# Performance work log

Measured on AMD Instinct MI355X. Metric: run time of the kernel, lower is better.

The kernel has to match this reference:

```python
import jax, jax.numpy as jnp
import numpy as np
from jax import lax

DILATIONS = [1, 2, 4, 8, 16, 32, 64, 128, 256, 512] * 2  # 20 layers
C = 128   # residual channels
K = 2     # kernel size


def _causal_dilated_conv(x, w, b, d):
    # x: [B, C, T], w: [2C, C, K], left-pad by d*(K-1) for causality
    pad = d * (K - 1)
    y = lax.conv_general_dilated(
        x, w, window_strides=(1,), padding=[(pad, 0)],
        rhs_dilation=(d,), dimension_numbers=('NCH', 'OIH', 'NCH'))
    return y + b[None, :, None]


def setup_inputs() -> dict:
    key = jax.random.key(0)
    ks = jax.random.split(key, 5)
    L = len(DILATIONS)
    x = jax.random.normal(ks[0], (4, C, 8192), jnp.float32)
    # 0.05 scale keeps activations stable through 20 residual layers
    w_conv = jax.random.normal(ks[1], (L, 2 * C, C, K), jnp.float32) * 0.05
    b_conv = jax.random.normal(ks[2], (L, 2 * C), jnp.float32) * 0.05
    w_out = jax.random.normal(ks[3], (L, C, C), jnp.float32) * 0.05
    b_out = jax.random.normal(ks[4], (L, C), jnp.float32) * 0.05
    return {"x": x, "w_conv": w_conv, "b_conv": b_conv,
            "w_out": w_out, "b_out": b_out}


def reference(x, w_conv, b_conv, w_out, b_out):
    """WaveNet convolution stack: per layer, causal dilated conv -> gated
    tanh*sigmoid -> 1x1 output conv; residual add; collect skips.
    Returns (output [B,C,T], skips [L,B,C,T])."""
    skips = []
    for i, d in enumerate(DILATIONS):
        h = x
        z = _causal_dilated_conv(x, w_conv[i], b_conv[i], d)  # [B, 2C, T]
        g = jnp.tanh(z[:, :C]) * jax.nn.sigmoid(z[:, C:])      # gated, [B, C, T]
        s = jnp.einsum('oc,bct->bot', w_out[i], g) + b_out[i][None, :, None]
        x = s + h  # residual connection
        skips.append(s)
    return x, jnp.stack(skips)
```

## Files before the change

kernel.cpp:

```cpp
#include <hip/hip_runtime.h>
#include <hip/hip_bf16.h>
#include <stdint.h>

using f32x4  = __attribute__((ext_vector_type(4))) float;
using bf16x8 = __attribute__((ext_vector_type(8))) short;
using bf16x4 = __attribute__((ext_vector_type(4))) short;

#define NB   4
#define NC   128
#define NT   8192
#define TL   64
#define NLAYER 20
#define GROWB 272
#define CONVN (NLAYER * 256 * 256)
#define WOUTN (NLAYER * 128 * 128)

__device__ __forceinline__ short f2b(float f) {
  union { float f; unsigned u; } v; v.f = f;
  unsigned r = v.u + 0x7FFFu + ((v.u >> 16) & 1u);
  return (short)(r >> 16);
}

__device__ __forceinline__ float b2f(short s) {
  union { unsigned u; float f; } v;
  v.u = ((unsigned)(unsigned short)s) << 16;
  return v.f;
}

__device__ __forceinline__ f32x4 mfma16(bf16x8 a, bf16x8 b, f32x4 c) {
  return __builtin_amdgcn_mfma_f32_16x16x32_bf16(a, b, c, 0, 0, 0);
}

__device__ __forceinline__ void gl_lds16(const void* g, void* l) {
  __builtin_amdgcn_global_load_lds(
      (const __attribute__((address_space(1))) void*)g,
      (__attribute__((address_space(3))) void*)l, 16, 0, 0);
}

__global__ void transpose_in(const float* __restrict__ x, short* __restrict__ xtb) {
  __shared__ float tile[64][65];
  const int t0 = blockIdx.x * 64;
  const int c0 = blockIdx.y * 64;
  const int b  = blockIdx.z;
  const int lane = threadIdx.x & 63;
  const int r4   = threadIdx.x >> 6;
  #pragma unroll
  for (int i = 0; i < 16; ++i) {
    const int cl = i * 4 + r4;
    tile[cl][lane] = x[((size_t)(b * NC + c0 + cl)) * NT + t0 + lane];
  }
  __syncthreads();
  #pragma unroll
  for (int it = 0; it < 2; ++it) {
    const int idx = it * 256 + threadIdx.x;
    const int r  = idx >> 3;
    const int gi = idx & 7;
    bf16x8 v;
    #pragma unroll
    for (int jj = 0; jj < 8; ++jj) v[jj] = f2b(tile[gi * 8 + jj][r]);
    const int t = t0 + r;
    const int ci = ((c0 >> 3) + gi) ^ (t & 7);
    *(bf16x8*)((char*)xtb + ((size_t)(b * NT + t)) * 256 + ci * 16) = v;
  }
}

__global__ void pack_weights(const float* __restrict__ w_conv,
                             const float* __restrict__ w_out,
                             short* __restrict__ wcb, short* __restrict__ wob) {
  const int idx = blockIdx.x * 256 + threadIdx.x;
  if (idx < CONVN) {
    const int k = idx & 255, o = (idx >> 8) & 255, lyr = idx >> 16;
    const int tap = k >> 7, c = k & 127;
    wcb[idx] = f2b(w_conv[(((size_t)lyr * 256 + o) * 128 + c) * 2 + tap]);
  } else if (idx < CONVN + WOUTN) {
    const int j = idx - CONVN;
    wob[j] = f2b(w_out[j]);
  }
}

__global__ __launch_bounds__(512, 4)
void wavenet_pair(const short* __restrict__ wcb,
                  const float* __restrict__ b_conv,
                  const short* __restrict__ wob,
                  const float* __restrict__ b_out,
                  const short* __restrict__ xbin,
                  short* __restrict__ xbout,
                  float* __restrict__ out,
                  int L, int d1, int d2)
{
  __shared__ char ldsY[80 * 256];
  __shared__ char ldsXG[88 * 256 + 80 * 256];
  char* X = ldsXG;
  char* G = ldsXG + 88 * 256;
  char* S = ldsXG;

  const int tid = threadIdx.x;
  const int w = tid >> 6, l = tid & 63, lh = l & 15, lq = l >> 4;
  const int o0 = 16 * w + lq * 4;
  const int uid = (blockIdx.x & 7) * 64 + (blockIdx.x >> 3);
  const int b   = uid >> 7;
  const int t0  = (uid & 127) * 64;
  const bool zhalo = (t0 == 0);
  const f32x4 fz = {0.f, 0.f, 0.f, 0.f};
  const size_t XOFFS = (size_t)NB * NC * NT;

  if (!zhalo) {
    const char* src = (const char*)xbin + ((size_t)(b * NT + t0 - 24)) * 256;
    #pragma unroll
    for (int k = 0; k < 3; ++k) {
      const int off = k * 8192 + tid * 16;
      if (off < 88 * 256) gl_lds16(src + off, X + off);
    }
  } else {
    if (tid * 16 < 6144) {
      bf16x8 z = {0, 0, 0, 0, 0, 0, 0, 0};
      *(bf16x8*)(X + tid * 16) = z;
    }
    const char* src = (const char*)xbin + ((size_t)(b * NT)) * 256;
    gl_lds16(src + tid * 16,        X + 6144 + tid * 16);
    gl_lds16(src + tid * 16 + 8192, X + 6144 + tid * 16 + 8192);
  }
  __syncthreads();

  f32x4 acc1[2][5];
  #pragma unroll
  for (int mi = 0; mi < 2; ++mi)
    #pragma unroll
    for (int nn = 0; nn < 5; ++nn) acc1[mi][nn] = fz;
  {
    const short* wl = wcb + (size_t)L * 65536;
    #pragma unroll
    for (int ks = 0; ks < 8; ++ks) {
      const bf16x8 a0 = *(const bf16x8*)(wl + (16 * w + lh) * 256 + ks * 32 + lq * 8);
      const bf16x8 a1 = *(const bf16x8*)(wl + (128 + 16 * w + lh) * 256 + ks * 32 + lq * 8);
      const int dd = (ks < 4) ? d1 : 0;
      #pragma unroll
      for (int nn = 0; nn < 5; ++nn) {
        const int p = 8 + nn * 16 + lh - dd;
        const int ci = ((ks & 3) * 4 + lq) ^ (p & 7);
        const bf16x8 bb = *(const bf16x8*)(X + p * 256 + ci * 16);
        acc1[0][nn] = mfma16(a0, bb, acc1[0][nn]);
        acc1[1][nn] = mfma16(a1, bb, acc1[1][nn]);
      }
    }
  }
  {
    float ba[4], bs[4];
    #pragma unroll
    for (int r = 0; r < 4; ++r) {
      ba[r] = b_conv[L * 256 + o0 + r];
      bs[r] = b_conv[L * 256 + 128 + o0 + r];
    }
    #pragma unroll
    for (int nn = 0; nn < 5; ++nn) {
      bf16x4 g4;
      #pragma unroll
      for (int r = 0; r < 4; ++r) {
        const float za = acc1[0][nn][r] + ba[r];
        const float zb = acc1[1][nn][r] + bs[r];
        const float th = 1.f - 2.f / (1.f + __expf(2.f * za));
        const float sg = 1.f / (1.f + __expf(-zb));
        g4[r] = f2b(th * sg);
      }
      const int q = nn * 16 + lh;
      const int ci = (o0 >> 3) ^ (q & 7);
      *(bf16x4*)(G + q * 256 + ci * 16 + (o0 & 7) * 2) = g4;
    }
  }
  __syncthreads();

  f32x4 s4vL[4];
  {
    f32x4 acc2[5];
    #pragma unroll
    for (int nn = 0; nn < 5; ++nn) acc2[nn] = fz;
    const short* wol = wob + (size_t)L * 16384;
    #pragma unroll
    for (int ks = 0; ks < 4; ++ks) {
      const bf16x8 a = *(const bf16x8*)(wol + (16 * w + lh) * 128 + ks * 32 + lq * 8);
      #pragma unroll
      for (int nn = 0; nn < 5; ++nn) {
        const int q = nn * 16 + lh;
        const int ci = (ks * 4 + lq) ^ (q & 7);
        const bf16x8 bb = *(const bf16x8*)(G + q * 256 + ci * 16);
        acc2[nn] = mfma16(a, bb, acc2[nn]);
      }
    }
    float bo[4];
    #pragma unroll
    for (int r = 0; r < 4; ++r) bo[r] = b_out[L * 128 + o0 + r];
    #pragma unroll
    for (int nn = 0; nn < 5; ++nn) {
      const int q = nn * 16 + lh;
      const int p = q + 8;
      const int ci = (o0 >> 3) ^ (q & 7);
      const bf16x4 h4 = *(const bf16x4*)(X + p * 256 + ci * 16 + (o0 & 7) * 2);
      f32x4 s4, xn;
      #pragma unroll
      for (int r = 0; r < 4; ++r) {
        s4[r] = acc2[nn][r] + bo[r];
        xn[r] = s4[r] + b2f(h4[r]);
      }
      if (nn >= 1) s4vL[nn - 1] = s4;
      bf16x4 x4;
      #pragma unroll
      for (int r = 0; r < 4; ++r) x4[r] = f2b(xn[r]);
      if (zhalo && nn == 0) { x4[0] = 0; x4[1] = 0; x4[2] = 0; x4[3] = 0; }
      *(bf16x4*)(ldsY + q * 256 + ci * 16 + (o0 & 7) * 2) = x4;
    }
  }
  __syncthreads();

  #pragma unroll
  for (int nn = 0; nn < 4; ++nn) {
    const int tt = nn * 16 + lh;
    #pragma unroll
    for (int r = 0; r < 4; ++r) {
      const int o  = o0 + r;
      const int lg = tt >> 2;
      const int pg = (lg & 8) | ((lg ^ (o & 7)) & 7);
      *(float*)(S + o * 256 + pg * 16 + (tt & 3) * 4) = s4vL[nn][r];
    }
  }
  __syncthreads();

  f32x4 acc1b[2][4];
  #pragma unroll
  for (int mi = 0; mi < 2; ++mi)
    #pragma unroll
    for (int n = 0; n < 4; ++n) acc1b[mi][n] = fz;
  {
    float* skipBase = out + XOFFS + ((size_t)((L * NB + b) * NC)) * NT + t0;
    const int j8 = tid & 7;
    #pragma unroll
    for (int half = 0; half < 2; ++half) {
      const int o = half * 64 + (tid >> 3);
      #pragma unroll
      for (int k = 0; k < 2; ++k) {
        const int pg = (k * 8) | ((j8 ^ (o & 7)) & 7);
        const f32x4 v = *(const f32x4*)(S + o * 256 + pg * 16);
        __builtin_nontemporal_store(v, (f32x4*)(skipBase + (size_t)o * NT + j8 * 4 + k * 32));
      }
    }
    const short* wl2 = wcb + (size_t)(L + 1) * 65536;
    #pragma unroll
    for (int ks = 0; ks < 8; ++ks) {
      const bf16x8 a0 = *(const bf16x8*)(wl2 + (16 * w + lh) * 256 + ks * 32 + lq * 8);
      const bf16x8 a1 = *(const bf16x8*)(wl2 + (128 + 16 * w + lh) * 256 + ks * 32 + lq * 8);
      const int dd = (ks < 4) ? d2 : 0;
      #pragma unroll
      for (int n = 0; n < 4; ++n) {
        const int qy = 16 + n * 16 + lh - dd;
        const int ci = ((ks & 3) * 4 + lq) ^ (qy & 7);
        const bf16x8 bb = *(const bf16x8*)(ldsY + qy * 256 + ci * 16);
        acc1b[0][n] = mfma16(a0, bb, acc1b[0][n]);
        acc1b[1][n] = mfma16(a1, bb, acc1b[1][n]);
      }
    }
  }
  __syncthreads();

  {
    float ba[4], bs[4];
    #pragma unroll
    for (int r = 0; r < 4; ++r) {
      ba[r] = b_conv[(L + 1) * 256 + o0 + r];
      bs[r] = b_conv[(L + 1) * 256 + 128 + o0 + r];
    }
    #pragma unroll
    for (int n = 0; n < 4; ++n) {
      bf16x4 g4;
      #pragma unroll
      for (int r = 0; r < 4; ++r) {
        const float za = acc1b[0][n][r] + ba[r];
        const float zb = acc1b[1][n][r] + bs[r];
        const float th = 1.f - 2.f / (1.f + __expf(2.f * za));
        const float sg = 1.f / (1.f + __expf(-zb));
        g4[r] = f2b(th * sg);
      }
      const int q2 = n * 16 + lh;
      const int ci = (o0 >> 3) ^ (q2 & 7);
      *(bf16x4*)(G + q2 * 256 + ci * 16 + (o0 & 7) * 2) = g4;
    }
  }
  __syncthreads();

  f32x4 s4vP[4];
  {
    f32x4 acc2[4];
    #pragma unroll
    for (int n = 0; n < 4; ++n) acc2[n] = fz;
    const short* wol2 = wob + (size_t)(L + 1) * 16384;
    #pragma unroll
    for (int ks = 0; ks < 4; ++ks) {
      const bf16x8 a = *(const bf16x8*)(wol2 + (16 * w + lh) * 128 + ks * 32 + lq * 8);
      #pragma unroll
      for (int n = 0; n < 4; ++n) {
        const int q2 = n * 16 + lh;
        const int ci = (ks * 4 + lq) ^ (q2 & 7);
        const bf16x8 bb = *(const bf16x8*)(G + q2 * 256 + ci * 16);
        acc2[n] = mfma16(a, bb, acc2[n]);
      }
    }
    float bo[4];
    #pragma unroll
    for (int r = 0; r < 4; ++r) bo[r] = b_out[(L + 1) * 128 + o0 + r];
    #pragma unroll
    for (int n = 0; n < 4; ++n) {
      const int q = 16 + n * 16 + lh;
      const int ci = (o0 >> 3) ^ (q & 7);
      const bf16x4 h4 = *(const bf16x4*)(ldsY + q * 256 + ci * 16 + (o0 & 7) * 2);
      f32x4 s4, xn;
      #pragma unroll
      for (int r = 0; r < 4; ++r) {
        s4[r] = acc2[n][r] + bo[r];
        xn[r] = s4[r] + b2f(h4[r]);
      }
      s4vP[n] = s4;
      bf16x4 x4;
      #pragma unroll
      for (int r = 0; r < 4; ++r) x4[r] = f2b(xn[r]);
      *(bf16x4*)(ldsY + q * 256 + ci * 16 + (o0 & 7) * 2) = x4;
    }
  }
  __syncthreads();

  #pragma unroll
  for (int n = 0; n < 4; ++n) {
    const int tt = n * 16 + lh;
    #pragma unroll
    for (int r = 0; r < 4; ++r) {
      const int o  = o0 + r;
      const int lg = tt >> 2;
      const int pg = (lg & 8) | ((lg ^ (o & 7)) & 7);
      *(float*)(S + o * 256 + pg * 16 + (tt & 3) * 4) = s4vP[n][r];
    }
  }
  __syncthreads();

  {
    float* skipBase = out + XOFFS + ((size_t)(((L + 1) * NB + b) * NC)) * NT + t0;
    const int j8 = tid & 7;
    #pragma unroll
    for (int half = 0; half < 2; ++half) {
      const int o = half * 64 + (tid >> 3);
      #pragma unroll
      for (int k = 0; k < 2; ++k) {
        const int pg = (k * 8) | ((j8 ^ (o & 7)) & 7);
        const f32x4 v = *(const f32x4*)(S + o * 256 + pg * 16);
        __builtin_nontemporal_store(v, (f32x4*)(skipBase + (size_t)o * NT + j8 * 4 + k * 32));
      }
    }
    char* dstBase = (char*)xbout + ((size_t)(b * NT + t0)) * 256;
    #pragma unroll
    for (int k = 0; k < 2; ++k) {
      const int idx = k * 512 + tid;
      const int r = idx >> 4, pcol = idx & 15;
      *(f32x4*)(dstBase + r * 256 + pcol * 16) =
          *(const f32x4*)(ldsY + (16 + r) * 256 + pcol * 16);
    }
  }
}

__global__ __launch_bounds__(512, 4)
void wavenet_layer(const short* __restrict__ wcb,
                   const float* __restrict__ b_conv,
                   const short* __restrict__ wob,
                   const float* __restrict__ b_out,
                   const short* __restrict__ xbin,
                   short* __restrict__ xbout,
                   float* __restrict__ out,
                   int layer, int dil, int last)
{
  __shared__ char ldsXC[TL * 256];
  __shared__ char ldsSP[TL * 256 + TL * GROWB];
  char* ldsXP = ldsSP;
  char* ldsG  = ldsSP + TL * 256;
  char* ldsS  = ldsSP;

  const int tid = threadIdx.x;
  const int w   = tid >> 6;
  const int l   = tid & 63;
  const int lh  = l & 15;
  const int lq  = l >> 4;
  const int o0  = 16 * w + lq * 4;
  const int uid = (blockIdx.x & 7) * 64 + (blockIdx.x >> 3);
  const int b   = uid >> 7;
  const int t0  = (uid & 127) * 64;

  {
    const char* xcg = (const char*)xbin + ((size_t)(b * NT + t0)) * 256;
    const int off = w * 2048 + l * 16;
    gl_lds16(xcg + off, ldsXC + off);
    gl_lds16(xcg + off + 1024, ldsXC + off + 1024);
  }
  if (t0 >= dil) {
    const char* xpg = (const char*)xbin + ((size_t)(b * NT + t0 - dil)) * 256;
    const int off = w * 2048 + l * 16;
    gl_lds16(xpg + off, ldsXP + off);
    gl_lds16(xpg + off + 1024, ldsXP + off + 1024);
  } else {
    const int row = tid >> 3, j8 = tid & 7;
    const int tp = t0 + row - dil;
    char* dst = ldsXP + row * 256;
    if (tp >= 0) {
      const char* src = (const char*)xbin + ((size_t)(b * NT + tp)) * 256;
      *(bf16x8*)(dst + j8 * 16)       = *(const bf16x8*)(src + j8 * 16);
      *(bf16x8*)(dst + j8 * 16 + 128) = *(const bf16x8*)(src + j8 * 16 + 128);
    } else {
      bf16x8 z = {0, 0, 0, 0, 0, 0, 0, 0};
      *(bf16x8*)(dst + j8 * 16)       = z;
      *(bf16x8*)(dst + j8 * 16 + 128) = z;
    }
  }
  __syncthreads();

  const f32x4 fz = {0.f, 0.f, 0.f, 0.f};
  f32x4 acc1[2][4];
  #pragma unroll
  for (int mi = 0; mi < 2; ++mi)
    #pragma unroll
    for (int n = 0; n < 4; ++n) acc1[mi][n] = fz;

  const short* wl = wcb + (size_t)layer * 65536;
  #pragma unroll
  for (int ks = 0; ks < 8; ++ks) {
    const bf16x8 a0 = *(const bf16x8*)(wl + (16 * w + lh) * 256 + ks * 32 + lq * 8);
    const bf16x8 a1 = *(const bf16x8*)(wl + (128 + 16 * w + lh) * 256 + ks * 32 + lq * 8);
    const char* base = (ks < 4) ? ldsXP : ldsXC;
    const int dd = (ks < 4) ? dil : 0;
    #pragma unroll
    for (int n = 0; n < 4; ++n) {
      const int tt = n * 16 + lh;
      const int ci = ((ks & 3) * 4 + lq) ^ ((tt - dd) & 7);
      const bf16x8 bb = *(const bf16x8*)(base + tt * 256 + ci * 16);
      acc1[0][n] = mfma16(a0, bb, acc1[0][n]);
      acc1[1][n] = mfma16(a1, bb, acc1[1][n]);
    }
  }

  {
    float ba[4], bs[4];
    #pragma unroll
    for (int r = 0; r < 4; ++r) {
      ba[r] = b_conv[layer * 256 + o0 + r];
      bs[r] = b_conv[layer * 256 + 128 + o0 + r];
    }
    #pragma unroll
    for (int n = 0; n < 4; ++n) {
      bf16x4 g4;
      #pragma unroll
      for (int r = 0; r < 4; ++r) {
        const float za = acc1[0][n][r] + ba[r];
        const float zb = acc1[1][n][r] + bs[r];
        const float th = 1.f - 2.f / (1.f + __expf(2.f * za));
        const float sg = 1.f / (1.f + __expf(-zb));
        g4[r] = f2b(th * sg);
      }
      const int tt = n * 16 + lh;
      *(bf16x4*)(ldsG + tt * GROWB + o0 * 2) = g4;
    }
  }
  __syncthreads();

  f32x4 acc2[4];
  #pragma unroll
  for (int n = 0; n < 4; ++n) acc2[n] = fz;
  const short* wol = wob + (size_t)layer * 16384;
  #pragma unroll
  for (int ks = 0; ks < 4; ++ks) {
    const bf16x8 a = *(const bf16x8*)(wol + (16 * w + lh) * 128 + ks * 32 + lq * 8);
    #pragma unroll
    for (int n = 0; n < 4; ++n) {
      const int tt = n * 16 + lh;
      const bf16x8 bb = *(const bf16x8*)(ldsG + tt * GROWB + ks * 64 + lq * 16);
      acc2[n] = mfma16(a, bb, acc2[n]);
    }
  }
  __syncthreads();

  f32x4 xn4[4];
  {
    float bo[4];
    #pragma unroll
    for (int r = 0; r < 4; ++r) bo[r] = b_out[layer * 128 + o0 + r];
    #pragma unroll
    for (int n = 0; n < 4; ++n) {
      const int tt = n * 16 + lh;
      const int ci = (o0 >> 3) ^ (tt & 7);
      const bf16x4 h4 = *(const bf16x4*)(ldsXC + tt * 256 + ci * 16 + (o0 & 7) * 2);
      f32x4 s4, xn;
      #pragma unroll
      for (int r = 0; r < 4; ++r) {
        s4[r] = acc2[n][r] + bo[r];
        xn[r] = s4[r] + b2f(h4[r]);
      }
      #pragma unroll
      for (int r = 0; r < 4; ++r) {
        const int o  = o0 + r;
        const int lg = tt >> 2;
        const int pg = (lg & 8) | ((lg ^ (o & 7)) & 7);
        *(float*)(ldsS + o * 256 + pg * 16 + (tt & 3) * 4) = s4[r];
      }
      if (!last) {
        bf16x4 x4;
        #pragma unroll
        for (int r = 0; r < 4; ++r) x4[r] = f2b(xn[r]);
        *(bf16x4*)(ldsXC + tt * 256 + ci * 16 + (o0 & 7) * 2) = x4;
      } else {
        xn4[n] = xn;
      }
    }
  }
  __syncthreads();

  const size_t XOFFS = (size_t)NB * NC * NT;
  {
    float* skipBase = out + XOFFS + ((size_t)((layer * NB + b) * NC)) * NT + t0;
    const int j8 = tid & 7;
    #pragma unroll
    for (int half = 0; half < 2; ++half) {
      const int o = half * 64 + (tid >> 3);
      #pragma unroll
      for (int k = 0; k < 2; ++k) {
        const int pg = (k * 8) | ((j8 ^ (o & 7)) & 7);
        const f32x4 v = *(const f32x4*)(ldsS + o * 256 + pg * 16);
        __builtin_nontemporal_store(v, (f32x4*)(skipBase + (size_t)o * NT + j8 * 4 + k * 32));
      }
    }
  }
  if (!last) {
    char* dstBase = (char*)xbout + ((size_t)(b * NT + t0)) * 256;
    #pragma unroll
    for (int k = 0; k < 2; ++k) {
      const int idx = k * 512 + tid;
      const int r = idx >> 4, p = idx & 15;
      *(f32x4*)(dstBase + r * 256 + p * 16) = *(const f32x4*)(ldsXC + r * 256 + p * 16);
    }
  } else {
    {
      #pragma unroll
      for (int n = 0; n < 4; ++n) {
        const int tt = n * 16 + lh;
        #pragma unroll
        for (int r = 0; r < 4; ++r)
          *(short*)(ldsXC + (o0 + r) * 128 + tt * 2) = f2b(xn4[n][r]);
      }
    }
    __syncthreads();
    float* xBase = out + ((size_t)(b * NC)) * NT + t0;
    const int j16 = tid & 15;
    #pragma unroll
    for (int k = 0; k < 4; ++k) {
      const int o = k * 32 + (tid >> 4);
      const bf16x4 v = *(const bf16x4*)(ldsXC + o * 128 + j16 * 8);
      f32x4 f;
      #pragma unroll
      for (int r = 0; r < 4; ++r) f[r] = b2f(v[r]);
      __builtin_nontemporal_store(f, (f32x4*)(xBase + (size_t)o * NT + j16 * 4));
    }
  }
}

extern "C" void kernel_launch(void* const* d_in, const int* in_sizes, int n_in,
                              void* d_out, int out_size, void* d_ws, size_t ws_size,
                              hipStream_t stream) {
  const float* x      = (const float*)d_in[0];
  const float* w_conv = (const float*)d_in[1];
  const float* b_conv = (const float*)d_in[2];
  const float* w_out  = (const float*)d_in[3];
  const float* b_out  = (const float*)d_in[4];
  float* out = (float*)d_out;

  const size_t XTN = (size_t)NB * NT * NC;
  short* xb[2];
  xb[0] = (short*)d_ws;
  xb[1] = xb[0] + XTN;
  short* wcb = xb[1] + XTN;
  short* wob = wcb + CONVN;

  pack_weights<<<(CONVN + WOUTN + 255) / 256, 256, 0, stream>>>(w_conv, w_out, wcb, wob);
  transpose_in<<<dim3(NT / 64, NC / 64, NB), 256, 0, stream>>>(x, xb[0]);

  int cur = 0;
  wavenet_pair<<<dim3(512), 512, 0, stream>>>(wcb, b_conv, wob, b_out,
                                              xb[cur], xb[cur ^ 1], out, 0, 1, 2);
  cur ^= 1;
  wavenet_pair<<<dim3(512), 512, 0, stream>>>(wcb, b_conv, wob, b_out,
                                              xb[cur], xb[cur ^ 1], out, 2, 4, 8);
  cur ^= 1;
  for (int i = 4; i <= 9; ++i) {
    wavenet_layer<<<dim3(512), 512, 0, stream>>>(
        wcb, b_conv, wob, b_out, xb[cur], xb[cur ^ 1], out, i, 1 << i, 0);
    cur ^= 1;
  }
  wavenet_pair<<<dim3(512), 512, 0, stream>>>(wcb, b_conv, wob, b_out,
                                              xb[cur], xb[cur ^ 1], out, 10, 1, 2);
  cur ^= 1;
  wavenet_pair<<<dim3(512), 512, 0, stream>>>(wcb, b_conv, wob, b_out,
                                              xb[cur], xb[cur ^ 1], out, 12, 4, 8);
  cur ^= 1;
  for (int i = 14; i <= 19; ++i) {
    wavenet_layer<<<dim3(512), 512, 0, stream>>>(
        wcb, b_conv, wob, b_out, xb[cur], xb[cur ^ 1], out, i, 1 << (i - 10),
        (i == 19) ? 1 : 0);
    cur ^= 1;
  }
}
```

Before: 353.0 us.

## Fuse dilation-16/32 layer pairs into one kernel with recomputed halo

Adds a wavenet_pair6 kernel that runs two consecutive layers (dilations 16 and 32) in one launch. It loads a 112-row halo and recomputes the first layer over 96 timesteps so the second layer's causal taps are available locally. This removes one global round trip of the bf16 activation tensor and one launch per pair, at the cost of 50% extra first-layer compute, more LDS, and extra register pressure.

```diff
diff --git a/kernel.cpp b/kernel.cpp
--- a/kernel.cpp
+++ b/kernel.cpp
@@ -358,6 +358,291 @@
       const int r = idx >> 4, pcol = idx & 15;
       *(f32x4*)(dstBase + r * 256 + pcol * 16) =
           *(const f32x4*)(ldsY + (16 + r) * 256 + pcol * 16);
+    }
+  }
+}
+
+__global__ __launch_bounds__(512, 4)
+void wavenet_pair6(const short* __restrict__ wcb,
+                   const float* __restrict__ b_conv,
+                   const short* __restrict__ wob,
+                   const float* __restrict__ b_out,
+                   const short* __restrict__ xbin,
+                   short* __restrict__ xbout,
+                   float* __restrict__ out,
+                   int L, int d1, int d2)
+{
+  __shared__ char ldsY[96 * 256];
+  __shared__ char ldsXG[112 * 256 + 96 * 256];
+  char* X = ldsXG;
+  char* G = ldsXG + 112 * 256;
+  char* S = ldsXG;
+
+  const int tid = threadIdx.x;
+  const int w = tid >> 6, l = tid & 63, lh = l & 15, lq = l >> 4;
+  const int o0 = 16 * w + lq * 4;
+  const int uid = (blockIdx.x & 7) * 64 + (blockIdx.x >> 3);
+  const int b   = uid >> 7;
+  const int t0  = (uid & 127) * 64;
+  const bool zhalo = (t0 == 0);
+  const f32x4 fz = {0.f, 0.f, 0.f, 0.f};
+  const size_t XOFFS = (size_t)NB * NC * NT;
+
+  if (!zhalo) {
+    const char* src = (const char*)xbin + ((size_t)(b * NT + t0 - 48)) * 256;
+    #pragma unroll
+    for (int k = 0; k < 4; ++k) {
+      const int off = k * 8192 + tid * 16;
+      if (off < 112 * 256) gl_lds16(src + off, X + off);
+    }
+  } else {
+    if (tid * 16 < 12288) {
+      bf16x8 z = {0, 0, 0, 0, 0, 0, 0, 0};
+      *(bf16x8*)(X + tid * 16) = z;
+      if (tid * 16 + 8192 < 12288) *(bf16x8*)(X + tid * 16 + 8192) = z;
+    }
+    const char* src = (const char*)xbin + ((size_t)(b * NT)) * 256;
+    gl_lds16(src + tid * 16,        X + 12288 + tid * 16);
+    gl_lds16(src + tid * 16 + 8192, X + 12288 + tid * 16 + 8192);
+  }
+  __syncthreads();
+
+  f32x4 acc1[2][6];
+  #pragma unroll
+  for (int mi = 0; mi < 2; ++mi)
+    #pragma unroll
+    for (int nn = 0; nn < 6; ++nn) acc1[mi][nn] = fz;
+  {
+    const short* wl = wcb + (size_t)L * 65536;
+    #pragma unroll
+    for (int ks = 0; ks < 8; ++ks) {
+      const bf16x8 a0 = *(const bf16x8*)(wl + (16 * w + lh) * 256 + ks * 32 + lq * 8);
+      const bf16x8 a1 = *(const bf16x8*)(wl + (128 + 16 * w + lh) * 256 + ks * 32 + lq * 8);
+      const int dd = (ks < 4) ? d1 : 0;
+      #pragma unroll
+      for (int nn = 0; nn < 6; ++nn) {
+        const int p = 16 + nn * 16 + lh - dd;
+        const int ci = ((ks & 3) * 4 + lq) ^ (p & 7);
+        const bf16x8 bb = *(const bf16x8*)(X + p * 256 + ci * 16);
+        acc1[0][nn] = mfma16(a0, bb, acc1[0][nn]);
+        acc1[1][nn] = mfma16(a1, bb, acc1[1][nn]);
+      }
+    }
+  }
+  {
+    float ba[4], bs[4];
+    #pragma unroll
+    for (int r = 0; r < 4; ++r) {
+      ba[r] = b_conv[L * 256 + o0 + r];
+      bs[r] = b_conv[L * 256 + 128 + o0 + r];
+    }
+    #pragma unroll
+    for (int nn = 0; nn < 6; ++nn) {
+      bf16x4 g4;
+      #pragma unroll
+      for (int r = 0; r < 4; ++r) {
+        const float za = acc1[0][nn][r] + ba[r];
+        const float zb = acc1[1][nn][r] + bs[r];
+        const float th = 1.f - 2.f / (1.f + __expf(2.f * za));
+        const float sg = 1.f / (1.f + __expf(-zb));
+        g4[r] = f2b(th * sg);
+      }
+      const int q = nn * 16 + lh;
+      const int ci = (o0 >> 3) ^ (q & 7);
+      *(bf16x4*)(G + q * 256 + ci * 16 + (o0 & 7) * 2) = g4;
+    }
+  }
+  __syncthreads();
+
+  f32x4 s4vL[4];
+  {
+    f32x4 acc2[6];
+    #pragma unroll
+    for (int nn = 0; nn < 6; ++nn) acc2[nn] = fz;
+    const short* wol = wob + (size_t)L * 16384;
+    #pragma unroll
+    for (int ks = 0; ks < 4; ++ks) {
+      const bf16x8 a = *(const bf16x8*)(wol + (16 * w + lh) * 128 + ks * 32 + lq * 8);
+      #pragma unroll
+      for (int nn = 0; nn < 6; ++nn) {
+        const int q = nn * 16 + lh;
+        const int ci = (ks * 4 + lq) ^ (q & 7);
+        const bf16x8 bb = *(const bf16x8*)(G + q * 256 + ci * 16);
+        acc2[nn] = mfma16(a, bb, acc2[nn]);
+      }
+    }
+    float bo[4];
+    #pragma unroll
+    for (int r = 0; r < 4; ++r) bo[r] = b_out[L * 128 + o0 + r];
+    #pragma unroll
+    for (int nn = 0; nn < 6; ++nn) {
+      const int q = nn * 16 + lh;
+      const int p = q + 16;
+      const int ci = (o0 >> 3) ^ (q & 7);
+      const bf16x4 h4 = *(const bf16x4*)(X + p * 256 + ci * 16 + (o0 & 7) * 2);
+      f32x4 s4, xn;
+      #pragma unroll
+      for (int r = 0; r < 4; ++r) {
+        s4[r] = acc2[nn][r] + bo[r];
+        xn[r] = s4[r] + b2f(h4[r]);
+      }
+      if (nn >= 2) s4vL[nn - 2] = s4;
+      bf16x4 x4;
+      #pragma unroll
+      for (int r = 0; r < 4; ++r) x4[r] = f2b(xn[r]);
+      if (zhalo && nn < 2) { x4[0] = 0; x4[1] = 0; x4[2] = 0; x4[3] = 0; }
+      *(bf16x4*)(ldsY + q * 256 + ci * 16 + (o0 & 7) * 2) = x4;
+    }
+  }
+  __syncthreads();
+
+  #pragma unroll
+  for (int nn = 0; nn < 4; ++nn) {
+    const int tt = nn * 16 + lh;
+    #pragma unroll
+    for (int r = 0; r < 4; ++r) {
+      const int o  = o0 + r;
+      const int lg = tt >> 2;
+      const int pg = (lg & 8) | ((lg ^ (o & 7)) & 7);
+      *(float*)(S + o * 256 + pg * 16 + (tt & 3) * 4) = s4vL[nn][r];
+    }
+  }
+  __syncthreads();
+
+  f32x4 acc1b[2][4];
+  #pragma unroll
+  for (int mi = 0; mi < 2; ++mi)
+    #pragma unroll
+    for (int n = 0; n < 4; ++n) acc1b[mi][n] = fz;
+  {
+    float* skipBase = out + XOFFS + ((size_t)((L * NB + b) * NC)) * NT + t0;
+    const int j8 = tid & 7;
+    #pragma unroll
+    for (int half = 0; half < 2; ++half) {
+      const int o = half * 64 + (tid >> 3);
+      #pragma unroll
+      for (int k = 0; k < 2; ++k) {
+        const int pg = (k * 8) | ((j8 ^ (o & 7)) & 7);
+        const f32x4 v = *(const f32x4*)(S + o * 256 + pg * 16);
+        __builtin_nontemporal_store(v, (f32x4*)(skipBase + (size_t)o * NT + j8 * 4 + k * 32));
+      }
+    }
+    const short* wl2 = wcb + (size_t)(L + 1) * 65536;
+    #pragma unroll
+    for (int ks = 0; ks < 8; ++ks) {
+      const bf16x8 a0 = *(const bf16x8*)(wl2 + (16 * w + lh) * 256 + ks * 32 + lq * 8);
+      const bf16x8 a1 = *(const bf16x8*)(wl2 + (128 + 16 * w + lh) * 256 + ks * 32 + lq * 8);
+      const int dd = (ks < 4) ? d2 : 0;
+      #pragma unroll
+      for (int n = 0; n < 4; ++n) {
+        const int qy = 32 + n * 16 + lh - dd;
+        const int ci = ((ks & 3) * 4 + lq) ^ (qy & 7);
+        const bf16x8 bb = *(const bf16x8*)(ldsY + qy * 256 + ci * 16);
+        acc1b[0][n] = mfma16(a0, bb, acc1b[0][n]);
+        acc1b[1][n] = mfma16(a1, bb, acc1b[1][n]);
+      }
+    }
+  }
+  __syncthreads();
+
+  {
+    float ba[4], bs[4];
+    #pragma unroll
+    for (int r = 0; r < 4; ++r) {
+      ba[r] = b_conv[(L + 1) * 256 + o0 + r];
+      bs[r] = b_conv[(L + 1) * 256 + 128 + o0 + r];
+    }
+    #pragma unroll
+    for (int n = 0; n < 4; ++n) {
+      bf16x4 g4;
+      #pragma unroll
+      for (int r = 0; r < 4; ++r) {
+        const float za = acc1b[0][n][r] + ba[r];
+        const float zb = acc1b[1][n][r] + bs[r];
+        const float th = 1.f - 2.f / (1.f + __expf(2.f * za));
+        const float sg = 1.f / (1.f + __expf(-zb));
+        g4[r] = f2b(th * sg);
+      }
+      const int q2 = n * 16 + lh;
+      const int ci = (o0 >> 3) ^ (q2 & 7);
+      *(bf16x4*)(G + q2 * 256 + ci * 16 + (o0 & 7) * 2) = g4;
+    }
+  }
+  __syncthreads();
+
+  f32x4 s4vP[4];
+  {
+    f32x4 acc2[4];
+    #pragma unroll
+    for (int n = 0; n < 4; ++n) acc2[n] = fz;
+    const short* wol2 = wob + (size_t)(L + 1) * 16384;
+    #pragma unroll
+    for (int ks = 0; ks < 4; ++ks) {
+      const bf16x8 a = *(const bf16x8*)(wol2 + (16 * w + lh) * 128 + ks * 32 + lq * 8);
+      #pragma unroll
+      for (int n = 0; n < 4; ++n) {
+        const int q2 = n * 16 + lh;
+        const int ci = (ks * 4 + lq) ^ (q2 & 7);
+        const bf16x8 bb = *(const bf16x8*)(G + q2 * 256 + ci * 16);
+        acc2[n] = mfma16(a, bb, acc2[n]);
+      }
+    }
+    float bo[4];
+    #pragma unroll
+    for (int r = 0; r < 4; ++r) bo[r] = b_out[(L + 1) * 128 + o0 + r];
+    #pragma unroll
+    for (int n = 0; n < 4; ++n) {
+      const int q = 32 + n * 16 + lh;
+      const int ci = (o0 >> 3) ^ (q & 7);
+      const bf16x4 h4 = *(const bf16x4*)(ldsY + q * 256 + ci * 16 + (o0 & 7) * 2);
+      f32x4 s4, xn;
+      #pragma unroll
+      for (int r = 0; r < 4; ++r) {
+        s4[r] = acc2[n][r] + bo[r];
+        xn[r] = s4[r] + b2f(h4[r]);
+      }
+      s4vP[n] = s4;
+      bf16x4 x4;
+      #pragma unroll
+      for (int r = 0; r < 4; ++r) x4[r] = f2b(xn[r]);
+      *(bf16x4*)(ldsY + q * 256 + ci * 16 + (o0 & 7) * 2) = x4;
+    }
+  }
+  __syncthreads();
+
+  #pragma unroll
+  for (int n = 0; n < 4; ++n) {
+    const int tt = n * 16 + lh;
+    #pragma unroll
+    for (int r = 0; r < 4; ++r) {
+      const int o  = o0 + r;
+      const int lg = tt >> 2;
+      const int pg = (lg & 8) | ((lg ^ (o & 7)) & 7);
+      *(float*)(S + o * 256 + pg * 16 + (tt & 3) * 4) = s4vP[n][r];
+    }
+  }
+  __syncthreads();
+
+  {
+    float* skipBase = out + XOFFS + ((size_t)(((L + 1) * NB + b) * NC)) * NT + t0;
+    const int j8 = tid & 7;
+    #pragma unroll
+    for (int half = 0; half < 2; ++half) {
+      const int o = half * 64 + (tid >> 3);
+      #pragma unroll
+      for (int k = 0; k < 2; ++k) {
+        const int pg = (k * 8) | ((j8 ^ (o & 7)) & 7);
+        const f32x4 v = *(const f32x4*)(S + o * 256 + pg * 16);
+        __builtin_nontemporal_store(v, (f32x4*)(skipBase + (size_t)o * NT + j8 * 4 + k * 32));
+      }
+    }
+    char* dstBase = (char*)xbout + ((size_t)(b * NT + t0)) * 256;
+    #pragma unroll
+    for (int k = 0; k < 2; ++k) {
+      const int idx = k * 512 + tid;
+      const int r = idx >> 4, pcol = idx & 15;
+      *(f32x4*)(dstBase + r * 256 + pcol * 16) =
+          *(const f32x4*)(ldsY + (32 + r) * 256 + pcol * 16);
     }
   }
 }
@@ -589,7 +874,10 @@
   wavenet_pair<<<dim3(512), 512, 0, stream>>>(wcb, b_conv, wob, b_out,
                                               xb[cur], xb[cur ^ 1], out, 2, 4, 8);
   cur ^= 1;
-  for (int i = 4; i <= 9; ++i) {
+  wavenet_pair6<<<dim3(512), 512, 0, stream>>>(wcb, b_conv, wob, b_out,
+                                               xb[cur], xb[cur ^ 1], out, 4, 16, 32);
+  cur ^= 1;
+  for (int i = 6; i <= 9; ++i) {
     wavenet_layer<<<dim3(512), 512, 0, stream>>>(
         wcb, b_conv, wob, b_out, xb[cur], xb[cur ^ 1], out, i, 1 << i, 0);
     cur ^= 1;
@@ -600,7 +888,10 @@
   wavenet_pair<<<dim3(512), 512, 0, stream>>>(wcb, b_conv, wob, b_out,
                                               xb[cur], xb[cur ^ 1], out, 12, 4, 8);
   cur ^= 1;
-  for (int i = 14; i <= 19; ++i) {
+  wavenet_pair6<<<dim3(512), 512, 0, stream>>>(wcb, b_conv, wob, b_out,
+                                               xb[cur], xb[cur ^ 1], out, 14, 16, 32);
+  cur ^= 1;
+  for (int i = 16; i <= 19; ++i) {
     wavenet_layer<<<dim3(512), 512, 0, stream>>>(
         wcb, b_conv, wob, b_out, xb[cur], xb[cur ^ 1], out, i, 1 << (i - 10),
         (i == 19) ? 1 : 0);
```

Measured after the change: 347.0 us. No clear change (-1.7%).
